# Optimization experiments

Measured on AMD Instinct MI355X. Metric: run time of the kernel, lower is better.

The kernel has to match this reference:

```python
import jax, jax.numpy as jnp
import numpy as np

SCALE = 8.0  # sqrt(head_dim=64)


def setup_inputs() -> dict:
    key = jax.random.key(0)
    k1, k2, k3, k4 = jax.random.split(key, 4)
    B, Lq, Lk, H, C, K = 2, 4096, 4096, 8, 64, 32
    return {
        "query": jax.random.normal(k1, (B, Lq, H, C), dtype=jnp.float32),
        "key": jax.random.normal(k2, (B, Lk, H, C), dtype=jnp.float32),
        "value": jax.random.normal(k3, (B, Lk, H, C), dtype=jnp.float32),
        "pos": jax.random.randint(k4, (B, Lq, H, K), 0, Lk, dtype=jnp.int64),
    }


def reference(query, key, value, pos):
    # query: [B, Lq, H, C]; key/value: [B, Lk, H, C]; pos: [B, Lq, H, K]
    B, Lq, H, C = query.shape
    b_idx = jnp.arange(B)[:, None, None, None]   # [B,1,1,1]
    h_idx = jnp.arange(H)[None, None, :, None]   # [1,1,H,1]
    # gather along sequence dim per (batch, head): -> [B, Lq, H, K, C]
    k = key[b_idx, pos, h_idx, :]
    v = value[b_idx, pos, h_idx, :]
    # per-query attention over K gathered keys
    score = jnp.einsum("blhc,blhkc->blhk", query, k) / SCALE
    attn = jax.nn.softmax(score, axis=-1)
    out = jnp.einsum("blhk,blhkc->blhc", attn, v)
    return out
```

## Files before the change

kernel.cpp:

```cpp
#include <hip/hip_runtime.h>
#include <math.h>

constexpr int B  = 2;
constexpr int Lq = 4096;
constexpr int Lk = 4096;
constexpr int H  = 8;
constexpr int C  = 64;
constexpr int K  = 32;
constexpr float INV_SCALE = 0.125f;
constexpr int HC = H * C;
constexpr int NKV = B * Lk * H * C;

typedef _Float16 half4_t __attribute__((ext_vector_type(4)));

__global__ __launch_bounds__(256) void convert_kv_f16(
    const float* __restrict__ key,
    const float* __restrict__ value,
    _Float16*    __restrict__ kh,
    _Float16*    __restrict__ vh)
{
    const int n4 = NKV / 4;
    for (int i = blockIdx.x * blockDim.x + threadIdx.x;
         i < 2 * n4; i += gridDim.x * blockDim.x) {
        if (i < n4) {
            const float4 v = ((const float4*)key)[i];
            half4_t h = { (_Float16)v.x, (_Float16)v.y, (_Float16)v.z, (_Float16)v.w };
            ((half4_t*)kh)[i] = h;
        } else {
            const float4 v = ((const float4*)value)[i - n4];
            half4_t h = { (_Float16)v.x, (_Float16)v.y, (_Float16)v.z, (_Float16)v.w };
            ((half4_t*)vh)[i - n4] = h;
        }
    }
}

__global__ __launch_bounds__(256) void topk_attn_f16(
    const float*    __restrict__ query,
    const _Float16* __restrict__ keyh,
    const _Float16* __restrict__ valh,
    const int*      __restrict__ pos,
    float*          __restrict__ out)
{
    const int bid    = blockIdx.x;
    const int group  = bid & 15;
    const int lchunk = bid >> 4;
    const int wave   = threadIdx.x >> 6;
    const int lane   = threadIdx.x & 63;
    const int g      = lane >> 4;
    const int c4     = lane & 15;

    const int b = group >> 3;
    const int h = group & 7;
    const int l = lchunk * 4 + wave;

    const size_t row  = ((size_t)(b * Lq + l) * H + h);
    const size_t qoff = row * (size_t)C;

    float4 q4 = *(const float4*)(query + qoff + 4 * c4);
    q4.x *= INV_SCALE; q4.y *= INV_SCALE; q4.z *= INV_SCALE; q4.w *= INV_SCALE;

    const int p = pos[row * (size_t)K + (lane & 31)];

    const _Float16* kbase = keyh + (size_t)b * Lk * HC + (size_t)h * C;
    const _Float16* vbase = valh + (size_t)b * Lk * HC + (size_t)h * C;

    int off[8];
    #pragma unroll
    for (int i = 0; i < 8; ++i)
        off[i] = __shfl(p, 4 * i + g) * HC + 4 * c4;

    float s[8];
    #pragma unroll
    for (int i = 0; i < 8; ++i) {
        const half4_t kv = *(const half4_t*)(kbase + off[i]);
        float t = q4.x * (float)kv.x;
        t = fmaf(q4.y, (float)kv.y, t);
        t = fmaf(q4.z, (float)kv.z, t);
        t = fmaf(q4.w, (float)kv.w, t);
        #pragma unroll
        for (int m = 8; m >= 1; m >>= 1) t += __shfl_xor(t, m);
        s[i] = t;
    }

    float mx = s[0];
    #pragma unroll
    for (int i = 1; i < 8; ++i) mx = fmaxf(mx, s[i]);
    mx = fmaxf(mx, __shfl_xor(mx, 16));
    mx = fmaxf(mx, __shfl_xor(mx, 32));

    float se = 0.0f;
    #pragma unroll
    for (int i = 0; i < 8; ++i) { s[i] = __expf(s[i] - mx); se += s[i]; }
    se += __shfl_xor(se, 16);
    se += __shfl_xor(se, 32);
    const float inv = 1.0f / se;

    float4 acc = make_float4(0.f, 0.f, 0.f, 0.f);
    #pragma unroll
    for (int i = 0; i < 8; ++i) {
        const float a = s[i] * inv;
        const half4_t v4 = *(const half4_t*)(vbase + off[i]);
        acc.x = fmaf(a, (float)v4.x, acc.x);
        acc.y = fmaf(a, (float)v4.y, acc.y);
        acc.z = fmaf(a, (float)v4.z, acc.z);
        acc.w = fmaf(a, (float)v4.w, acc.w);
    }
    #pragma unroll
    for (int m = 16; m <= 32; m <<= 1) {
        acc.x += __shfl_xor(acc.x, m);
        acc.y += __shfl_xor(acc.y, m);
        acc.z += __shfl_xor(acc.z, m);
        acc.w += __shfl_xor(acc.w, m);
    }

    if (g == 0) *(float4*)(out + qoff + 4 * c4) = acc;
}

__global__ __launch_bounds__(256) void topk_attn_f32(
    const float* __restrict__ query,
    const float* __restrict__ key,
    const float* __restrict__ value,
    const int*   __restrict__ pos,
    float*       __restrict__ out)
{
    const int bid    = blockIdx.x;
    const int group  = bid & 15;
    const int lchunk = bid >> 4;
    const int wave   = threadIdx.x >> 6;
    const int lane   = threadIdx.x & 63;
    const int g      = lane >> 4;
    const int c4     = lane & 15;

    const int b = group >> 3;
    const int h = group & 7;
    const int l = lchunk * 4 + wave;

    const size_t row  = ((size_t)(b * Lq + l) * H + h);
    const size_t qoff = row * (size_t)C;

    float4 q4 = *(const float4*)(query + qoff + 4 * c4);
    q4.x *= INV_SCALE; q4.y *= INV_SCALE; q4.z *= INV_SCALE; q4.w *= INV_SCALE;

    const int p = pos[row * (size_t)K + (lane & 31)];

    const float* kbase = key   + (size_t)b * Lk * HC + (size_t)h * C;
    const float* vbase = value + (size_t)b * Lk * HC + (size_t)h * C;

    int off[8];
    #pragma unroll
    for (int i = 0; i < 8; ++i)
        off[i] = __shfl(p, 4 * i + g) * HC + 4 * c4;

    float s[8];
    #pragma unroll
    for (int i = 0; i < 8; ++i) {
        const float4 kv = *(const float4*)(kbase + off[i]);
        float t = q4.x * kv.x;
        t = fmaf(q4.y, kv.y, t);
        t = fmaf(q4.z, kv.z, t);
        t = fmaf(q4.w, kv.w, t);
        #pragma unroll
        for (int m = 8; m >= 1; m >>= 1) t += __shfl_xor(t, m);
        s[i] = t;
    }

    float mx = s[0];
    #pragma unroll
    for (int i = 1; i < 8; ++i) mx = fmaxf(mx, s[i]);
    mx = fmaxf(mx, __shfl_xor(mx, 16));
    mx = fmaxf(mx, __shfl_xor(mx, 32));

    float se = 0.0f;
    #pragma unroll
    for (int i = 0; i < 8; ++i) { s[i] = __expf(s[i] - mx); se += s[i]; }
    se += __shfl_xor(se, 16);
    se += __shfl_xor(se, 32);
    const float inv = 1.0f / se;

    float4 acc = make_float4(0.f, 0.f, 0.f, 0.f);
    #pragma unroll
    for (int i = 0; i < 8; ++i) {
        const float a = s[i] * inv;
        const float4 v4 = *(const float4*)(vbase + off[i]);
        acc.x = fmaf(a, v4.x, acc.x);
        acc.y = fmaf(a, v4.y, acc.y);
        acc.z = fmaf(a, v4.z, acc.z);
        acc.w = fmaf(a, v4.w, acc.w);
    }
    #pragma unroll
    for (int m = 16; m <= 32; m <<= 1) {
        acc.x += __shfl_xor(acc.x, m);
        acc.y += __shfl_xor(acc.y, m);
        acc.z += __shfl_xor(acc.z, m);
        acc.w += __shfl_xor(acc.w, m);
    }

    if (g == 0) *(float4*)(out + qoff + 4 * c4) = acc;
}

extern "C" void kernel_launch(void* const* d_in, const int* in_sizes, int n_in,
                              void* d_out, int out_size, void* d_ws, size_t ws_size,
                              hipStream_t stream) {
    const float* query = (const float*)d_in[0];
    const float* key   = (const float*)d_in[1];
    const float* value = (const float*)d_in[2];
    const int*   pos   = (const int*)d_in[3];
    float* out = (float*)d_out;

    const int total_rows = B * Lq * H;
    const int blocks = total_rows / 4;

    const size_t need = (size_t)2 * NKV * sizeof(_Float16);
    if (ws_size >= need && d_ws != nullptr) {
        _Float16* kh = (_Float16*)d_ws;
        _Float16* vh = kh + NKV;
        convert_kv_f16<<<2048, 256, 0, stream>>>(key, value, kh, vh);
        topk_attn_f16<<<blocks, 256, 0, stream>>>(query, kh, vh, pos, out);
    } else {
        topk_attn_f32<<<blocks, 256, 0, stream>>>(query, key, value, pos, out);
    }
}
```

Baseline: 53.16 us.

## Use 16-byte fp16 gathers with packed dot2 and half2 accumulation

Restructures the fp16 attention kernel so each lane handles 8 channels with 16-byte loads, and 8 lanes cover a row, so each lane makes 4 gathers instead of 8. Scores are computed with packed fp16 dot2 instructions, and the weighted value sum is accumulated in packed half2 with half2 shuffles. This cuts the number of memory instructions, shuffles and ALU ops per row. In exchange, the query and the softmax weights are rounded to fp16 and the output accumulates in fp16, which reduces accuracy.

```diff
diff --git a/kernel.cpp b/kernel.cpp
--- a/kernel.cpp
+++ b/kernel.cpp
@@ -11,7 +11,28 @@
 constexpr int HC = H * C;
 constexpr int NKV = B * Lk * H * C;
 
+typedef _Float16 h2 __attribute__((ext_vector_type(2)));
 typedef _Float16 half4_t __attribute__((ext_vector_type(4)));
+
+static __device__ __forceinline__ h2 pack_h2(float lo, float hi) {
+    return __builtin_bit_cast(h2, __builtin_amdgcn_cvt_pkrtz(lo, hi));
+}
+
+#if __has_builtin(__builtin_amdgcn_fdot2)
+static __device__ __forceinline__ float fdot2(h2 a, h2 b, float c) {
+    return __builtin_amdgcn_fdot2(a, b, c, false);
+}
+#else
+static __device__ __forceinline__ float fdot2(h2 a, h2 b, float c) {
+    return c + (float)a.x * (float)b.x + (float)a.y * (float)b.y;
+}
+#endif
+
+static __device__ __forceinline__ h2 shfl_h2_xor(h2 v, int m) {
+    int i = __builtin_bit_cast(int, v);
+    i = __shfl_xor(i, m);
+    return __builtin_bit_cast(h2, i);
+}
 
 __global__ __launch_bounds__(256) void convert_kv_f16(
     const float* __restrict__ key,
@@ -46,8 +67,8 @@
     const int lchunk = bid >> 4;
     const int wave   = threadIdx.x >> 6;
     const int lane   = threadIdx.x & 63;
-    const int g      = lane >> 4;
-    const int c4     = lane & 15;
+    const int g      = lane >> 3;
+    const int c8     = lane & 7;
 
     const int b = group >> 3;
     const int h = group & 7;
@@ -56,64 +77,81 @@
     const size_t row  = ((size_t)(b * Lq + l) * H + h);
     const size_t qoff = row * (size_t)C;
 
-    float4 q4 = *(const float4*)(query + qoff + 4 * c4);
-    q4.x *= INV_SCALE; q4.y *= INV_SCALE; q4.z *= INV_SCALE; q4.w *= INV_SCALE;
+    const float4 qa = *(const float4*)(query + qoff + 8 * c8);
+    const float4 qb = *(const float4*)(query + qoff + 8 * c8 + 4);
+    h2 qp[4];
+    qp[0] = pack_h2(qa.x * INV_SCALE, qa.y * INV_SCALE);
+    qp[1] = pack_h2(qa.z * INV_SCALE, qa.w * INV_SCALE);
+    qp[2] = pack_h2(qb.x * INV_SCALE, qb.y * INV_SCALE);
+    qp[3] = pack_h2(qb.z * INV_SCALE, qb.w * INV_SCALE);
 
     const int p = pos[row * (size_t)K + (lane & 31)];
 
     const _Float16* kbase = keyh + (size_t)b * Lk * HC + (size_t)h * C;
     const _Float16* vbase = valh + (size_t)b * Lk * HC + (size_t)h * C;
 
-    int off[8];
-    #pragma unroll
-    for (int i = 0; i < 8; ++i)
-        off[i] = __shfl(p, 4 * i + g) * HC + 4 * c4;
-
-    float s[8];
-    #pragma unroll
-    for (int i = 0; i < 8; ++i) {
-        const half4_t kv = *(const half4_t*)(kbase + off[i]);
-        float t = q4.x * (float)kv.x;
-        t = fmaf(q4.y, (float)kv.y, t);
-        t = fmaf(q4.z, (float)kv.z, t);
-        t = fmaf(q4.w, (float)kv.w, t);
+    int off[4];
+    #pragma unroll
+    for (int i = 0; i < 4; ++i)
+        off[i] = __shfl(p, 4 * g + i) * HC + 8 * c8;
+
+    float s[4];
+    #pragma unroll
+    for (int i = 0; i < 4; ++i) {
+        const uint4 kv = *(const uint4*)(kbase + off[i]);
+        float t = fdot2(qp[0], __builtin_bit_cast(h2, kv.x), 0.0f);
+        t = fdot2(qp[1], __builtin_bit_cast(h2, kv.y), t);
+        t = fdot2(qp[2], __builtin_bit_cast(h2, kv.z), t);
+        t = fdot2(qp[3], __builtin_bit_cast(h2, kv.w), t);
         #pragma unroll
-        for (int m = 8; m >= 1; m >>= 1) t += __shfl_xor(t, m);
+        for (int m = 4; m >= 1; m >>= 1) t += __shfl_xor(t, m);
         s[i] = t;
     }
 
-    float mx = s[0];
-    #pragma unroll
-    for (int i = 1; i < 8; ++i) mx = fmaxf(mx, s[i]);
+    float mx = fmaxf(fmaxf(s[0], s[1]), fmaxf(s[2], s[3]));
+    mx = fmaxf(mx, __shfl_xor(mx, 8));
     mx = fmaxf(mx, __shfl_xor(mx, 16));
     mx = fmaxf(mx, __shfl_xor(mx, 32));
 
     float se = 0.0f;
     #pragma unroll
-    for (int i = 0; i < 8; ++i) { s[i] = __expf(s[i] - mx); se += s[i]; }
+    for (int i = 0; i < 4; ++i) { s[i] = __expf(s[i] - mx); se += s[i]; }
+    se += __shfl_xor(se, 8);
     se += __shfl_xor(se, 16);
     se += __shfl_xor(se, 32);
     const float inv = 1.0f / se;
 
-    float4 acc = make_float4(0.f, 0.f, 0.f, 0.f);
-    #pragma unroll
-    for (int i = 0; i < 8; ++i) {
+    h2 a2[4];
+    #pragma unroll
+    for (int i = 0; i < 4; ++i) {
         const float a = s[i] * inv;
-        const half4_t v4 = *(const half4_t*)(vbase + off[i]);
-        acc.x = fmaf(a, (float)v4.x, acc.x);
-        acc.y = fmaf(a, (float)v4.y, acc.y);
-        acc.z = fmaf(a, (float)v4.z, acc.z);
-        acc.w = fmaf(a, (float)v4.w, acc.w);
-    }
-    #pragma unroll
-    for (int m = 16; m <= 32; m <<= 1) {
-        acc.x += __shfl_xor(acc.x, m);
-        acc.y += __shfl_xor(acc.y, m);
-        acc.z += __shfl_xor(acc.z, m);
-        acc.w += __shfl_xor(acc.w, m);
-    }
-
-    if (g == 0) *(float4*)(out + qoff + 4 * c4) = acc;
+        a2[i] = pack_h2(a, a);
+    }
+
+    h2 acc[4] = { h2{0,0}, h2{0,0}, h2{0,0}, h2{0,0} };
+    #pragma unroll
+    for (int i = 0; i < 4; ++i) {
+        const uint4 vv = *(const uint4*)(vbase + off[i]);
+        acc[0] = a2[i] * __builtin_bit_cast(h2, vv.x) + acc[0];
+        acc[1] = a2[i] * __builtin_bit_cast(h2, vv.y) + acc[1];
+        acc[2] = a2[i] * __builtin_bit_cast(h2, vv.z) + acc[2];
+        acc[3] = a2[i] * __builtin_bit_cast(h2, vv.w) + acc[3];
+    }
+    #pragma unroll
+    for (int m = 8; m <= 32; m <<= 1) {
+        #pragma unroll
+        for (int j = 0; j < 4; ++j)
+            acc[j] = acc[j] + shfl_h2_xor(acc[j], m);
+    }
+
+    if (g == 0) {
+        const float4 o0 = make_float4((float)acc[0].x, (float)acc[0].y,
+                                      (float)acc[1].x, (float)acc[1].y);
+        const float4 o1 = make_float4((float)acc[2].x, (float)acc[2].y,
+                                      (float)acc[3].x, (float)acc[3].y);
+        *(float4*)(out + qoff + 8 * c8)     = o0;
+        *(float4*)(out + qoff + 8 * c8 + 4) = o1;
+    }
 }
 
 __global__ __launch_bounds__(256) void topk_attn_f32(
```

New measurement: 47.26 us. 11.1% less time.
